# Kernel optimization log

Hardware: AMD Instinct MI355X
Metric: run time of the kernel (lower is better)

## Reference

```python
import jax, jax.numpy as jnp
import numpy as np

EMBED_DIM = 1024
NUM_HEADS = 16
HEAD_DIM = EMBED_DIM // NUM_HEADS
SCALE = HEAD_DIM ** -0.5


def setup_inputs() -> dict:
    key = jax.random.key(0)
    k1, k2, k3 = jax.random.split(key, 3)
    B, S, E = 2, 2048, EMBED_DIM
    # xavier-uniform-like init scaled down for stability
    x = jax.random.normal(k1, (B, S, E), dtype=jnp.float32)
    w_qkv = jax.random.normal(k2, (3 * E, E), dtype=jnp.float32) * (E ** -0.5)
    w_out = jax.random.normal(k3, (E, E), dtype=jnp.float32) * (E ** -0.5)
    bias_qkv = jnp.zeros((3 * E,), dtype=jnp.float32)
    bias_out = jnp.zeros((E,), dtype=jnp.float32)
    return {"x": x, "w_qkv": w_qkv, "bias_qkv": bias_qkv, "w_out": w_out, "bias_out": bias_out}


def reference(x, w_qkv, bias_qkv, w_out, bias_out):
    B, S, E = x.shape
    H, D = NUM_HEADS, HEAD_DIM
    # fused QKV projection: nn.Linear semantics -> x @ w_qkv.T + bias
    qkv = jnp.einsum('bse,fe->bsf', x, w_qkv) + bias_qkv  # [B,S,3E]
    q, k, v = jnp.split(qkv, 3, axis=-1)
    # reshape to heads
    q = q.reshape(B, S, H, D)
    k = k.reshape(B, S, H, D)
    v = v.reshape(B, S, H, D)
    # scaled dot-product attention (non-causal)
    scores = jnp.einsum('bqhd,bkhd->bhqk', q, k) * SCALE  # [B,H,S,S]
    probs = jax.nn.softmax(scores, axis=-1)
    ctx = jnp.einsum('bhqk,bkhd->bqhd', probs, v).reshape(B, S, E)
    # output projection
    out = jnp.einsum('bse,fe->bsf', ctx, w_out) + bias_out
    return out
```

## Files before the change

kernel.cpp:

```cpp
#include <hip/hip_runtime.h>
#include <hip/hip_bf16.h>


typedef __bf16 bf16_t;
typedef __bf16 bf16x4 __attribute__((ext_vector_type(4)));
typedef __bf16 bf16x8 __attribute__((ext_vector_type(8)));
typedef short s16x4 __attribute__((ext_vector_type(4)));
typedef float f32x4 __attribute__((ext_vector_type(4)));

#define MFMA16(a, b, c) __builtin_amdgcn_mfma_f32_16x16x32_bf16(a, b, c, 0, 0, 0)
#define MFMA16X16(a, b, c) __builtin_amdgcn_mfma_f32_16x16x16bf16_1k(a, b, c, 0, 0, 0)

static constexpr int Bn = 2;
static constexpr int S = 2048;
static constexpr int E = 1024;
static constexpr int H = 16;
static constexpr int Dh = 64;

__device__ __forceinline__ void gl_lds16(const bf16_t* g, bf16_t* l) {
  __builtin_amdgcn_global_load_lds(
      (const __attribute__((address_space(1))) unsigned int*)g,
      (__attribute__((address_space(3))) unsigned int*)l, 16, 0, 0);
}

__device__ __forceinline__ int detect_fp32(const unsigned short* p) {
  int cnt = 0;
#pragma unroll
  for (int j = 0; j < 32; j++) {
    const int e = (p[j] >> 7) & 0xFF;
    cnt += (e > 140) ? 1 : 0;
  }
  return cnt >= 2;
}

static constexpr int G0 = 4194304 / 8;
static constexpr int G1 = G0 + 3145728 / 8;
static constexpr int G2 = G1 + 3072 / 8;
static constexpr int G3 = G2 + 1048576 / 8;
static constexpr int G4 = G3 + 1024 / 8;

__global__ void convert_all(const void* __restrict__ s0, const void* __restrict__ s1,
                            const void* __restrict__ s2, const void* __restrict__ s3,
                            const void* __restrict__ s4, bf16_t* __restrict__ dst) {
  const int fp32 = detect_fp32((const unsigned short*)s0);
  const int stride = gridDim.x * blockDim.x;
  for (int i = blockIdx.x * blockDim.x + threadIdx.x; i < G4; i += stride) {
    const void* s;
    int off;
    if (i < G0)      { s = s0; off = i; }
    else if (i < G1) { s = s1; off = i - G0; }
    else if (i < G2) { s = s2; off = i - G1; }
    else if (i < G3) { s = s3; off = i - G2; }
    else             { s = s4; off = i - G3; }
    bf16x8 o;
    if (fp32) {
      const float* sp = (const float*)s + off * 8;
#pragma unroll
      for (int j = 0; j < 8; j++) o[j] = (bf16_t)sp[j];
    } else {
      o = *((const bf16x8*)s + off);
    }
    *(bf16x8*)(dst + (size_t)i * 8) = o;
  }
}

__global__ __launch_bounds__(256) void gemm_qkv(
    const bf16_t* __restrict__ X, const bf16_t* __restrict__ W,
    const bf16_t* __restrict__ bias,
    bf16_t* __restrict__ Qo, bf16_t* __restrict__ Ko, bf16_t* __restrict__ Vo) {
  __shared__ bf16_t Alds[16 * 512];
  __shared__ bf16_t Blds[16 * 512];
  const int tid = threadIdx.x;
  const int wave = tid >> 6, lane = tid & 63;
  const int lr = lane & 15, quad = lane >> 4;
  const int wm = wave >> 1, wn = wave & 1;
  const int m0 = blockIdx.y * 128, n0 = blockIdx.x * 128;
  constexpr int Kd = 1024;

  f32x4 acc[4][4] = {};
  for (int k0 = 0; k0 < Kd; k0 += 64) {
    __syncthreads();
#pragma unroll
    for (int i = 0; i < 4; i++) {
      const int fb = wave * 4 + i;
      const int mt = fb >> 1, kc = fb & 1;
      gl_lds16(X + (size_t)(m0 + mt * 16 + lr) * Kd + k0 + kc * 32 + quad * 8,
               &Alds[fb * 512]);
      gl_lds16(W + (size_t)(n0 + mt * 16 + lr) * Kd + k0 + kc * 32 + quad * 8,
               &Blds[fb * 512]);
    }
    __syncthreads();
#pragma unroll
    for (int kc = 0; kc < 2; kc++) {
      bf16x8 af[4], bfr[4];
#pragma unroll
      for (int mt = 0; mt < 4; mt++)
        af[mt] = *(const bf16x8*)&Alds[((wm * 4 + mt) * 2 + kc) * 512 + lane * 8];
#pragma unroll
      for (int nt = 0; nt < 4; nt++)
        bfr[nt] = *(const bf16x8*)&Blds[((wn * 4 + nt) * 2 + kc) * 512 + lane * 8];
#pragma unroll
      for (int mt = 0; mt < 4; mt++)
#pragma unroll
        for (int nt = 0; nt < 4; nt++)
          acc[mt][nt] = MFMA16(af[mt], bfr[nt], acc[mt][nt]);
    }
  }

  const int m0w = m0 + wm * 64, n0w = n0 + wn * 64;
#pragma unroll
  for (int nt = 0; nt < 4; nt++) {
    const int col = n0w + nt * 16 + lr;
    const float bs = (float)bias[col];
    const int which = col >> 10;
    const int e = col & 1023;
    const int h = e >> 6, d = e & 63;
#pragma unroll
    for (int mt = 0; mt < 4; mt++) {
      const int row0 = m0w + mt * 16 + quad * 4;
      const int b = row0 >> 11, s0 = row0 & 2047;
      if (which == 2) {
        bf16x4 v4;
#pragma unroll
        for (int r = 0; r < 4; r++) v4[r] = (bf16_t)(acc[mt][nt][r] + bs);
        *(bf16x4*)&Vo[((size_t)((b * H + h) * Dh + d)) * S + s0] = v4;
      } else {
        bf16_t* dst = (which == 0) ? Qo : Ko;
#pragma unroll
        for (int r = 0; r < 4; r++)
          dst[((size_t)((b * H + h) * S + (s0 + r))) * Dh + d] =
              (bf16_t)(acc[mt][nt][r] + bs);
      }
    }
  }
}

__global__ __launch_bounds__(256, 4) void attn_kernel(
    const bf16_t* __restrict__ Q, const bf16_t* __restrict__ K,
    const bf16_t* __restrict__ Vt, bf16_t* __restrict__ CTX) {
  __shared__ bf16_t Kl[8 * 512];
  __shared__ bf16_t Vl[8 * 512];

  const int tid = threadIdx.x;
  const int wave = tid >> 6, lane = tid & 63;
  const int lr = lane & 15, quad = lane >> 4;

  const int blk = blockIdx.x;
  const int bh = blk & 31;
  const int qt = blk >> 5;
  const int b = bh >> 4, h = bh & 15;

  const bf16_t* Qb = Q + (size_t)bh * S * Dh;
  const bf16_t* Kb = K + (size_t)bh * S * Dh;
  const bf16_t* Vb = Vt + (size_t)bh * Dh * S;

  const int q0 = qt * 64 + wave * 16;

  const bf16x8 aq0 = *(const bf16x8*)(Qb + (size_t)(q0 + lr) * Dh + quad * 8);
  const bf16x8 aq1 = *(const bf16x8*)(Qb + (size_t)(q0 + lr) * Dh + 32 + quad * 8);

  const bf16_t* kg = Kb + (size_t)(wave * 16 + lr) * Dh + quad * 8;
  const bf16_t* vg = Vb + (size_t)(wave * 16 + lr) * S + quad * 8;

  const int vq = ((quad >> 1) * 16 + lr) * 8 + (quad & 1) * 4;

  f32x4 O[4] = {};
  float lp = 0.f;

  for (int sk0 = 0; sk0 < S; sk0 += 64) {
    __syncthreads();
    gl_lds16(kg + (size_t)sk0 * Dh, &Kl[(wave * 2 + 0) * 512]);
    gl_lds16(kg + (size_t)sk0 * Dh + 32, &Kl[(wave * 2 + 1) * 512]);
    gl_lds16(vg + sk0, &Vl[(wave * 2 + 0) * 512]);
    gl_lds16(vg + sk0 + 32, &Vl[(wave * 2 + 1) * 512]);
    __syncthreads();

#pragma unroll
    for (int kt = 0; kt < 4; kt++) {
      const bf16x8 kf0 = *(const bf16x8*)&Kl[(kt * 2 + 0) * 512 + lane * 8];
      const bf16x8 kf1 = *(const bf16x8*)&Kl[(kt * 2 + 1) * 512 + lane * 8];
      f32x4 z = {};
      z = MFMA16(kf0, aq0, z);
      const f32x4 sc = MFMA16(kf1, aq1, z);

      bf16x4 pb;
      float ps = 0.f;
#pragma unroll
      for (int r = 0; r < 4; r++) {
        const float p = __expf(sc[r] * 0.125f);
        ps += p;
        pb[r] = (bf16_t)p;
      }
      lp += ps;
      const s16x4 pbi = __builtin_bit_cast(s16x4, pb);

      const int vbase = (kt >> 1) * 512 + ((kt & 1) * 256 + vq);
#pragma unroll
      for (int dt = 0; dt < 4; dt++) {
        const bf16x4 va = *(const bf16x4*)&Vl[dt * 1024 + vbase];
        O[dt] = MFMA16X16(__builtin_bit_cast(s16x4, va), pbi, O[dt]);
      }
    }
  }

  lp += __shfl_xor(lp, 16);
  lp += __shfl_xor(lp, 32);
  const float rl = 1.0f / lp;

  const int qrow = q0 + lr;
#pragma unroll
  for (int dt = 0; dt < 4; dt++) {
    bf16x4 o4;
#pragma unroll
    for (int r = 0; r < 4; r++) o4[r] = (bf16_t)(O[dt][r] * rl);
    *(bf16x4*)&CTX[(size_t)(b * S + qrow) * E + h * 64 + dt * 16 + quad * 4] = o4;
  }
}

__global__ __launch_bounds__(256) void gemm_out(
    const bf16_t* __restrict__ X, const bf16_t* __restrict__ W,
    const bf16_t* __restrict__ bias, void* __restrict__ Out,
    const void* __restrict__ xin) {
  __shared__ bf16_t Alds[8 * 512];
  __shared__ bf16_t Blds[16 * 512];
  const int tid = threadIdx.x;
  const int wave = tid >> 6, lane = tid & 63;
  const int lr = lane & 15, quad = lane >> 4;
  const int wm = wave >> 1, wn = wave & 1;
  const int m0 = blockIdx.y * 64, n0 = blockIdx.x * 128;
  constexpr int Kd = 1024;

  f32x4 acc[2][4] = {};
  for (int k0 = 0; k0 < Kd; k0 += 64) {
    __syncthreads();
#pragma unroll
    for (int kc = 0; kc < 2; kc++)
      gl_lds16(X + (size_t)(m0 + wave * 16 + lr) * Kd + k0 + kc * 32 + quad * 8,
               &Alds[(wave * 2 + kc) * 512]);
#pragma unroll
    for (int i = 0; i < 2; i++) {
      const int nt = wave * 2 + i;
#pragma unroll
      for (int kc = 0; kc < 2; kc++)
        gl_lds16(W + (size_t)(n0 + nt * 16 + lr) * Kd + k0 + kc * 32 + quad * 8,
                 &Blds[(nt * 2 + kc) * 512]);
    }
    __syncthreads();
#pragma unroll
    for (int kc = 0; kc < 2; kc++) {
      bf16x8 af[2], bfr[4];
#pragma unroll
      for (int mt = 0; mt < 2; mt++)
        af[mt] = *(const bf16x8*)&Alds[((wm * 2 + mt) * 2 + kc) * 512 + lane * 8];
#pragma unroll
      for (int nt = 0; nt < 4; nt++)
        bfr[nt] = *(const bf16x8*)&Blds[((wn * 4 + nt) * 2 + kc) * 512 + lane * 8];
#pragma unroll
      for (int mt = 0; mt < 2; mt++)
#pragma unroll
        for (int nt = 0; nt < 4; nt++)
          acc[mt][nt] = MFMA16(af[mt], bfr[nt], acc[mt][nt]);
    }
  }

  const int fp32 = detect_fp32((const unsigned short*)xin);
  const int m0w = m0 + wm * 32, n0w = n0 + wn * 64;
#pragma unroll
  for (int nt = 0; nt < 4; nt++) {
    const int col = n0w + nt * 16 + lr;
    const float bs = (float)bias[col];
#pragma unroll
    for (int mt = 0; mt < 2; mt++) {
#pragma unroll
      for (int r = 0; r < 4; r++) {
        const int row = m0w + mt * 16 + quad * 4 + r;
        const float v = acc[mt][nt][r] + bs;
        if (fp32)
          ((float*)Out)[(size_t)row * E + col] = v;
        else
          ((bf16_t*)Out)[(size_t)row * E + col] = (bf16_t)v;
      }
    }
  }
}

extern "C" void kernel_launch(void* const* d_in, const int* in_sizes, int n_in,
                              void* d_out, int out_size, void* d_ws, size_t ws_size,
                              hipStream_t stream) {
  const void* x = d_in[0];
  const void* w_qkv = d_in[1];
  const void* b_qkv = d_in[2];
  const void* w_out = d_in[3];
  const void* b_out = d_in[4];

  bf16_t* base = (bf16_t*)d_ws;
  const int N_X = Bn * S * E;
  const int N_WQ = 3 * E * E;
  const int N_BQ = 3 * E;
  const int N_WO = E * E;
  const int N_BO = E;
  bf16_t* xb = base;
  bf16_t* wqb = xb + N_X;
  bf16_t* bqb = wqb + N_WQ;
  bf16_t* wob = bqb + N_BQ;
  bf16_t* bob = wob + N_WO;
  const size_t QKV_ELEMS = (size_t)Bn * H * S * Dh;
  bf16_t* Qw = bob + N_BO;
  bf16_t* Kw = Qw + QKV_ELEMS;
  bf16_t* Vw = Kw + QKV_ELEMS;
  bf16_t* CTXw = Vw + QKV_ELEMS;

  convert_all<<<1024, 256, 0, stream>>>(x, w_qkv, b_qkv, w_out, b_out, xb);
  gemm_qkv<<<dim3(3 * E / 128, Bn * S / 128), 256, 0, stream>>>(xb, wqb, bqb, Qw, Kw, Vw);
  attn_kernel<<<32 * Bn * H, 256, 0, stream>>>(Qw, Kw, Vw, CTXw);
  gemm_out<<<dim3(E / 128, Bn * S / 64), 256, 0, stream>>>(CTXw, wob, bob, d_out, x);
}
```

Measured before the change: 229.3 us.

## Stage QKV epilogue through LDS for coalesced stores; double attention KV tile

The QKV GEMM epilogue now writes its biased tile into a padded shared-memory buffer, then writes Q/K rows and transposed V rows back to global memory as 16-byte vectors instead of scattered 2-byte and 8-byte stores. The attention kernel processes 128 keys per iteration instead of 64, halving the number of barriers per sweep at the cost of doubling K/V shared memory. The softmax exponent uses exp2f with a pre-folded log2e scale. The larger LDS footprint may limit occupancy against the 4-blocks launch bound.

```diff
diff --git a/kernel.cpp b/kernel.cpp
--- a/kernel.cpp
+++ b/kernel.cpp
@@ -68,8 +68,9 @@
     const bf16_t* __restrict__ X, const bf16_t* __restrict__ W,
     const bf16_t* __restrict__ bias,
     bf16_t* __restrict__ Qo, bf16_t* __restrict__ Ko, bf16_t* __restrict__ Vo) {
-  __shared__ bf16_t Alds[16 * 512];
-  __shared__ bf16_t Blds[16 * 512];
+  __shared__ bf16_t Smem[17408];
+  bf16_t* Alds = Smem;
+  bf16_t* Blds = Smem + 8192;
   const int tid = threadIdx.x;
   const int wave = tid >> 6, lane = tid & 63;
   const int lr = lane & 15, quad = lane >> 4;
@@ -107,30 +108,44 @@
     }
   }
 
-  const int m0w = m0 + wm * 64, n0w = n0 + wn * 64;
+  constexpr int LT = 136;
+  __syncthreads();
 #pragma unroll
   for (int nt = 0; nt < 4; nt++) {
-    const int col = n0w + nt * 16 + lr;
-    const float bs = (float)bias[col];
-    const int which = col >> 10;
-    const int e = col & 1023;
-    const int h = e >> 6, d = e & 63;
+    const int cl = wn * 64 + nt * 16 + lr;
+    const float bs = (float)bias[n0 + cl];
 #pragma unroll
     for (int mt = 0; mt < 4; mt++) {
-      const int row0 = m0w + mt * 16 + quad * 4;
-      const int b = row0 >> 11, s0 = row0 & 2047;
-      if (which == 2) {
-        bf16x4 v4;
-#pragma unroll
-        for (int r = 0; r < 4; r++) v4[r] = (bf16_t)(acc[mt][nt][r] + bs);
-        *(bf16x4*)&Vo[((size_t)((b * H + h) * Dh + d)) * S + s0] = v4;
-      } else {
-        bf16_t* dst = (which == 0) ? Qo : Ko;
-#pragma unroll
-        for (int r = 0; r < 4; r++)
-          dst[((size_t)((b * H + h) * S + (s0 + r))) * Dh + d] =
-              (bf16_t)(acc[mt][nt][r] + bs);
-      }
+      const int rl0 = wm * 64 + mt * 16 + quad * 4;
+#pragma unroll
+      for (int r = 0; r < 4; r++)
+        Smem[(rl0 + r) * LT + cl] = (bf16_t)(acc[mt][nt][r] + bs);
+    }
+  }
+  __syncthreads();
+
+  const int which = n0 >> 10;
+  const int b = m0 >> 11, s0g = m0 & 2047;
+  const int hA = (n0 & 1023) >> 6;
+  if (which < 2) {
+    bf16_t* dst = which ? Ko : Qo;
+    const int row = tid >> 1, half = tid & 1;
+    bf16_t* gp = dst + ((size_t)((b * H + hA + half) * S + s0g + row)) * Dh;
+    const bf16_t* tp = &Smem[row * LT + half * 64];
+#pragma unroll
+    for (int j = 0; j < 8; j++)
+      *(bf16x8*)(gp + j * 8) = *(const bf16x8*)(tp + j * 8);
+  } else {
+    const int col = tid >> 1, shalf = tid & 1;
+    const int d = col & 63, h = hA + (col >> 6);
+    bf16_t* gp = Vo + ((size_t)((b * H + h) * Dh + d)) * S + s0g + shalf * 64;
+#pragma unroll
+    for (int j8 = 0; j8 < 8; j8++) {
+      bf16x8 o;
+#pragma unroll
+      for (int j = 0; j < 8; j++)
+        o[j] = Smem[(shalf * 64 + j8 * 8 + j) * LT + col];
+      *(bf16x8*)(gp + j8 * 8) = o;
     }
   }
 }
@@ -138,8 +153,8 @@
 __global__ __launch_bounds__(256, 4) void attn_kernel(
     const bf16_t* __restrict__ Q, const bf16_t* __restrict__ K,
     const bf16_t* __restrict__ Vt, bf16_t* __restrict__ CTX) {
-  __shared__ bf16_t Kl[8 * 512];
-  __shared__ bf16_t Vl[8 * 512];
+  __shared__ bf16_t Kl[16 * 512];
+  __shared__ bf16_t Vl[16 * 512];
 
   const int tid = threadIdx.x;
   const int wave = tid >> 6, lane = tid & 63;
@@ -159,24 +174,28 @@
   const bf16x8 aq0 = *(const bf16x8*)(Qb + (size_t)(q0 + lr) * Dh + quad * 8);
   const bf16x8 aq1 = *(const bf16x8*)(Qb + (size_t)(q0 + lr) * Dh + 32 + quad * 8);
 
-  const bf16_t* kg = Kb + (size_t)(wave * 16 + lr) * Dh + quad * 8;
-  const bf16_t* vg = Vb + (size_t)(wave * 16 + lr) * S + quad * 8;
-
   const int vq = ((quad >> 1) * 16 + lr) * 8 + (quad & 1) * 4;
 
   f32x4 O[4] = {};
   float lp = 0.f;
-
-  for (int sk0 = 0; sk0 < S; sk0 += 64) {
-    __syncthreads();
-    gl_lds16(kg + (size_t)sk0 * Dh, &Kl[(wave * 2 + 0) * 512]);
-    gl_lds16(kg + (size_t)sk0 * Dh + 32, &Kl[(wave * 2 + 1) * 512]);
-    gl_lds16(vg + sk0, &Vl[(wave * 2 + 0) * 512]);
-    gl_lds16(vg + sk0 + 32, &Vl[(wave * 2 + 1) * 512]);
-    __syncthreads();
-
-#pragma unroll
-    for (int kt = 0; kt < 4; kt++) {
+  const float C = 0.125f * 1.44269504f;
+
+  for (int sk0 = 0; sk0 < S; sk0 += 128) {
+    __syncthreads();
+#pragma unroll
+    for (int i = 0; i < 4; i++) {
+      const int kt = wave * 2 + (i >> 1), kc = i & 1;
+      gl_lds16(Kb + (size_t)(sk0 + kt * 16 + lr) * Dh + kc * 32 + quad * 8,
+               &Kl[(kt * 2 + kc) * 512]);
+    }
+#pragma unroll
+    for (int kc = 0; kc < 4; kc++)
+      gl_lds16(Vb + (size_t)(wave * 16 + lr) * S + sk0 + kc * 32 + quad * 8,
+               &Vl[(wave * 4 + kc) * 512]);
+    __syncthreads();
+
+#pragma unroll
+    for (int kt = 0; kt < 8; kt++) {
       const bf16x8 kf0 = *(const bf16x8*)&Kl[(kt * 2 + 0) * 512 + lane * 8];
       const bf16x8 kf1 = *(const bf16x8*)&Kl[(kt * 2 + 1) * 512 + lane * 8];
       f32x4 z = {};
@@ -187,17 +206,17 @@
       float ps = 0.f;
 #pragma unroll
       for (int r = 0; r < 4; r++) {
-        const float p = __expf(sc[r] * 0.125f);
+        const float p = exp2f(sc[r] * C);
         ps += p;
         pb[r] = (bf16_t)p;
       }
       lp += ps;
       const s16x4 pbi = __builtin_bit_cast(s16x4, pb);
 
-      const int vbase = (kt >> 1) * 512 + ((kt & 1) * 256 + vq);
+      const int vbase = (kt >> 1) * 512 + (kt & 1) * 256 + vq;
 #pragma unroll
       for (int dt = 0; dt < 4; dt++) {
-        const bf16x4 va = *(const bf16x4*)&Vl[dt * 1024 + vbase];
+        const bf16x4 va = *(const bf16x4*)&Vl[dt * 2048 + vbase];
         O[dt] = MFMA16X16(__builtin_bit_cast(s16x4, va), pbi, O[dt]);
       }
     }
```

After: 249.8 us. +8.9%, slower.

## Double-buffer K/V LDS tiles in attention kernel and use exp2

Applied to the files above, without the earlier changes.

Doubles the K and V shared-memory tiles so the next tile's global-to-LDS load is issued before computing on the current tile. This cuts one barrier per iteration and hides load latency. The softmax exponent switches from __expf to exp2f with the log2e factor folded into the scale constant. LDS use per block doubles, which could reduce occupancy, and correctness depends on the asynchronous LDS loads being waited on before the barrier.

```diff
diff --git a/kernel.cpp b/kernel.cpp
--- a/kernel.cpp
+++ b/kernel.cpp
@@ -138,8 +138,8 @@
 __global__ __launch_bounds__(256, 4) void attn_kernel(
     const bf16_t* __restrict__ Q, const bf16_t* __restrict__ K,
     const bf16_t* __restrict__ Vt, bf16_t* __restrict__ CTX) {
-  __shared__ bf16_t Kl[8 * 512];
-  __shared__ bf16_t Vl[8 * 512];
+  __shared__ bf16_t Kl[2][8 * 512];
+  __shared__ bf16_t Vl[2][8 * 512];
 
   const int tid = threadIdx.x;
   const int wave = tid >> 6, lane = tid & 63;
@@ -166,19 +166,26 @@
 
   f32x4 O[4] = {};
   float lp = 0.f;
-
-  for (int sk0 = 0; sk0 < S; sk0 += 64) {
-    __syncthreads();
-    gl_lds16(kg + (size_t)sk0 * Dh, &Kl[(wave * 2 + 0) * 512]);
-    gl_lds16(kg + (size_t)sk0 * Dh + 32, &Kl[(wave * 2 + 1) * 512]);
-    gl_lds16(vg + sk0, &Vl[(wave * 2 + 0) * 512]);
-    gl_lds16(vg + sk0 + 32, &Vl[(wave * 2 + 1) * 512]);
-    __syncthreads();
+  const float C = 0.125f * 1.44269504f;
+
+  auto stage = [&](int bb, int sk) {
+    gl_lds16(kg + (size_t)sk * Dh, &Kl[bb][(wave * 2 + 0) * 512]);
+    gl_lds16(kg + (size_t)sk * Dh + 32, &Kl[bb][(wave * 2 + 1) * 512]);
+    gl_lds16(vg + sk, &Vl[bb][(wave * 2 + 0) * 512]);
+    gl_lds16(vg + sk + 32, &Vl[bb][(wave * 2 + 1) * 512]);
+  };
+
+  stage(0, 0);
+  __syncthreads();
+
+  for (int i = 0; i < S / 64; i++) {
+    const int cur = i & 1;
+    if (i + 1 < S / 64) stage(1 - cur, (i + 1) * 64);
 
 #pragma unroll
     for (int kt = 0; kt < 4; kt++) {
-      const bf16x8 kf0 = *(const bf16x8*)&Kl[(kt * 2 + 0) * 512 + lane * 8];
-      const bf16x8 kf1 = *(const bf16x8*)&Kl[(kt * 2 + 1) * 512 + lane * 8];
+      const bf16x8 kf0 = *(const bf16x8*)&Kl[cur][(kt * 2 + 0) * 512 + lane * 8];
+      const bf16x8 kf1 = *(const bf16x8*)&Kl[cur][(kt * 2 + 1) * 512 + lane * 8];
       f32x4 z = {};
       z = MFMA16(kf0, aq0, z);
       const f32x4 sc = MFMA16(kf1, aq1, z);
@@ -187,20 +194,22 @@
       float ps = 0.f;
 #pragma unroll
       for (int r = 0; r < 4; r++) {
-        const float p = __expf(sc[r] * 0.125f);
+        const float p = exp2f(sc[r] * C);
         ps += p;
         pb[r] = (bf16_t)p;
       }
       lp += ps;
       const s16x4 pbi = __builtin_bit_cast(s16x4, pb);
 
-      const int vbase = (kt >> 1) * 512 + ((kt & 1) * 256 + vq);
+      const int vbase = (kt >> 1) * 512 + (kt & 1) * 256 + vq;
 #pragma unroll
       for (int dt = 0; dt < 4; dt++) {
-        const bf16x4 va = *(const bf16x4*)&Vl[dt * 1024 + vbase];
+        const bf16x4 va = *(const bf16x4*)&Vl[cur][dt * 1024 + vbase];
         O[dt] = MFMA16X16(__builtin_bit_cast(s16x4, va), pbi, O[dt]);
       }
     }
+
+    __syncthreads();
   }
 
   lp += __shfl_xor(lp, 16);
```

Result: slower. 241.1 us (+5.1%).
